# Kernel tuning notes

Measured on AMD Instinct MI355X. Metric: run time of the kernel, lower is better.

## Reference

```python
import jax, jax.numpy as jnp
import numpy as np

B, N, C = 4, 4096, 256
GROUPS = 50
M_SCALE = 10.0


def setup_inputs() -> dict:
    key = jax.random.key(0)
    ks = jax.random.split(key, 6)
    s = 0.02
    return {
        "inputs": jax.random.normal(ks[0], (B, N, 1, C), dtype=jnp.float32),
        "W_sem": jax.random.normal(ks[1], (C, 128), dtype=jnp.float32) * s,
        "b_sem": jnp.zeros((128,), jnp.float32),
        "W_seg": jax.random.normal(ks[2], (128, GROUPS), dtype=jnp.float32) * s,
        "b_seg": jnp.zeros((GROUPS,), jnp.float32),
        "W_sim": jax.random.normal(ks[3], (C, 128), dtype=jnp.float32) * s,
        "b_sim": jnp.zeros((128,), jnp.float32),
        "W_conf": jax.random.normal(ks[4], (C, 128), dtype=jnp.float32) * s,
        "b_conf": jnp.zeros((128,), jnp.float32),
        "W_cl": jax.random.normal(ks[5], (128, 1), dtype=jnp.float32) * s,
        "b_cl": jnp.zeros((1,), jnp.float32),
    }


def reference(inputs, W_sem, b_sem, W_seg, b_seg, W_sim, b_sim,
              W_conf, b_conf, W_cl, b_cl):
    # 1x1 Conv2D on [B, N, 1, C] == per-point dense layer on channels.
    x = inputs[:, :, 0, :]  # [B, N, C]

    # Semantic segmentation head
    Fsem = jnp.einsum('bnc,cd->bnd', x, W_sem) + b_sem          # [B, N, 128]
    ptssemseg_logits = jnp.einsum('bnd,dg->bng', Fsem, W_seg) + b_seg  # [B, N, G]
    ptssemseg = jax.nn.softmax(ptssemseg_logits, axis=-1)

    # Similarity head: pairwise squared distances of Fsim rows
    Fsim = jnp.einsum('bnc,cd->bnd', x, W_sim) + b_sim          # [B, N, 128]
    r = jnp.sum(Fsim * Fsim, axis=2)                             # [B, N]
    gram = jnp.einsum('bnd,bmd->bnm', Fsim, Fsim)                # [B, N, N]
    D = r[:, :, None] - 2.0 * gram + r[:, None, :]               # [B, N, N]
    simmat_logits = jnp.maximum(M_SCALE * D, 0.0)

    # Confidence head
    Fconf = jnp.einsum('bnc,cd->bnd', x, W_conf) + b_conf        # [B, N, 128]
    conf_logits = jnp.einsum('bnd,do->bno', Fconf, W_cl) + b_cl  # [B, N, 1]
    conf = jax.nn.sigmoid(conf_logits)

    return (ptssemseg, ptssemseg_logits, simmat_logits, conf, conf_logits)
```

## Files before the change

### kernel.cpp

```cpp
#include <hip/hip_runtime.h>
#include <cstdint>
#include <cstddef>

#define NN 4096
#define CC 256
#define GG 50
#define PB 32
#define JD 384

#define O_OUT1 819200
#define O_OUT2 1638400
#define O_OUT3 68747264
#define O_OUT4 68763648

__device__ __forceinline__ unsigned bf16b(float f) {
    unsigned u = __float_as_uint(f);
    return (u + 0x7FFFu + ((u >> 16) & 1u)) >> 16;
}
__device__ __forceinline__ float bf16f(short s) {
    return __uint_as_float(((unsigned)(unsigned short)s) << 16);
}

__global__ __launch_bounds__(256) void k_proj(
    const float* __restrict__ x,
    const float* __restrict__ Wsem, const float* __restrict__ bsem,
    const float* __restrict__ Wseg, const float* __restrict__ bseg,
    const float* __restrict__ Wsim, const float* __restrict__ bsim,
    const float* __restrict__ Wconf, const float* __restrict__ bconf,
    const float* __restrict__ Wcl, const float* __restrict__ bcl,
    unsigned* __restrict__ fsimu, float* __restrict__ rnorm,
    float* __restrict__ out0, float* __restrict__ out1,
    float* __restrict__ out3, float* __restrict__ out4)
{
    __shared__ float smem[15360];
    __shared__ float confl[PB], mxs[PB], sms[PB], rns[PB];

    float* xs  = smem;
    float* wch = smem + 9216;

    int t = threadIdx.x;
    int pbase = blockIdx.x * PB;
    if (t < PB) { confl[t] = 0.f; rns[t] = 0.f; }

    #pragma unroll 4
    for (int p = 0; p < PB; ++p)
        xs[t * 36 + p] = x[(size_t)(pbase + p) * CC + t];

    int tj = t & 31, tp = t >> 5;
    float acc[4][12];
    #pragma unroll
    for (int pp = 0; pp < 4; ++pp)
        #pragma unroll
        for (int jj = 0; jj < 12; ++jj) acc[pp][jj] = 0.f;

    for (int kc = 0; kc < 16; ++kc) {
        __syncthreads();
        #pragma unroll
        for (int i = 0; i < 8; ++i) {
            int idx = i * 256 + t;
            int k = idx >> 7, jj = idx & 127;
            int g = (kc * 16 + k) * 128 + jj;
            wch[k * JD +       jj] = Wsim[g];
            wch[k * JD + 128 + jj] = Wsem[g];
            wch[k * JD + 256 + jj] = Wconf[g];
        }
        __syncthreads();
        #pragma unroll
        for (int k = 0; k < 16; ++k) {
            const float* xp = &xs[(kc * 16 + k) * 36 + tp * 4];
            float a0 = xp[0], a1 = xp[1], a2 = xp[2], a3 = xp[3];
            const float* wr = &wch[k * JD + tj * 12];
            #pragma unroll
            for (int jj = 0; jj < 12; ++jj) {
                float w = wr[jj];
                acc[0][jj] = fmaf(a0, w, acc[0][jj]);
                acc[1][jj] = fmaf(a1, w, acc[1][jj]);
                acc[2][jj] = fmaf(a2, w, acc[2][jj]);
                acc[3][jj] = fmaf(a3, w, acc[3][jj]);
            }
        }
    }
    __syncthreads();

    float* hsem = smem;
    float* WsT  = smem + 4224;
    float* segl = smem + 10824;

    for (int i = t; i < GG * 128; i += 256) {
        int g = i >> 7, d = i & 127;
        WsT[g * 132 + d] = Wseg[d * GG + g];
    }

    #pragma unroll
    for (int pp = 0; pp < 4; ++pp) {
        int p = tp * 4 + pp;
        float vv[12];
        #pragma unroll
        for (int jj = 0; jj < 12; ++jj) {
            int j = tj * 12 + jj;
            float bb = (j < 128) ? bsim[j] : (j < 256 ? bsem[j - 128] : bconf[j - 256]);
            vv[jj] = acc[pp][jj] + bb;
        }
        float rsq = 0.f;
        #pragma unroll
        for (int jj = 0; jj < 12; ++jj) {
            int j = tj * 12 + jj;
            if (j < 128) {
                float f = bf16f((short)bf16b(vv[jj]));
                rsq = fmaf(f, f, rsq);
            }
        }
        if (tj <= 10) atomicAdd(&rns[p], rsq);
        #pragma unroll
        for (int jj = 0; jj < 12; jj += 2) {
            int j = tj * 12 + jj;
            if (j < 128)
                fsimu[(size_t)(pbase + p) * 64 + (j >> 1)] =
                    bf16b(vv[jj]) | (bf16b(vv[jj + 1]) << 16);
        }
        #pragma unroll
        for (int jj = 0; jj < 12; ++jj) {
            int j = tj * 12 + jj;
            if (j >= 128 && j < 256) hsem[p * 132 + (j - 128)] = vv[jj];
        }
        float c = 0.f;
        #pragma unroll
        for (int jj = 0; jj < 12; ++jj) {
            int j = tj * 12 + jj;
            if (j >= 256) c = fmaf(vv[jj], Wcl[j - 256], c);
        }
        if (tj >= 21) atomicAdd(&confl[p], c);
    }
    __syncthreads();

    for (int i = t; i < PB * GG; i += 256) {
        int p = i / GG, g = i - p * GG;
        const float4* hp = (const float4*)&hsem[p * 132];
        const float4* wp = (const float4*)&WsT[g * 132];
        float a = bseg[g];
        #pragma unroll 8
        for (int d = 0; d < 32; ++d) {
            float4 h = hp[d], w = wp[d];
            a = fmaf(h.x, w.x, a); a = fmaf(h.y, w.y, a);
            a = fmaf(h.z, w.z, a); a = fmaf(h.w, w.w, a);
        }
        segl[p * 52 + g] = a;
    }
    __syncthreads();

    if (t < PB) {
        int p = t;
        float mx = -1e30f;
        for (int g = 0; g < GG; ++g) mx = fmaxf(mx, segl[p * 52 + g]);
        float s = 0.f;
        for (int g = 0; g < GG; ++g) s += __expf(segl[p * 52 + g] - mx);
        mxs[p] = mx; sms[p] = 1.f / s;
        float cl = confl[p] + bcl[0];
        out4[pbase + p] = cl;
        out3[pbase + p] = 1.f / (1.f + __expf(-cl));
        rnorm[pbase + p] = rns[p];
    }
    __syncthreads();

    for (int i = t; i < PB * GG; i += 256) {
        int p = i / GG, g = i - p * GG;
        float l = segl[p * 52 + g];
        size_t o = (size_t)(pbase + p) * GG + g;
        out1[o] = l;
        out0[o] = __expf(l - mxs[p]) * sms[p];
    }
}

typedef short short8 __attribute__((ext_vector_type(8)));
typedef float f32x4 __attribute__((ext_vector_type(4)));

__global__ __launch_bounds__(256) void k_simmat(
    const short* __restrict__ fs, const float* __restrict__ rn, float* __restrict__ out2)
{
    int t = threadIdx.x;
    int lane = t & 63, wv = t >> 6;
    int b = blockIdx.y;

    int p = blockIdx.x;
    int tj = (int)((sqrtf((float)(8 * p + 1)) - 1.f) * 0.5f);
    while ((tj + 1) * (tj + 2) / 2 <= p) ++tj;
    while (tj * (tj + 1) / 2 > p) --tj;
    int ti = p - tj * (tj + 1) / 2;

    int I = ti * 128 + (wv >> 1) * 64;
    int J = tj * 128 + (wv & 1) * 64;
    int rowl = lane & 15, quad = lane >> 4;

    const short8* F = (const short8*)(fs + (size_t)b * NN * 128);
    const float* rb = rn + b * NN;

    f32x4 acc[4][4];
    #pragma unroll
    for (int r = 0; r < 4; ++r)
        #pragma unroll
        for (int c = 0; c < 4; ++c) { f32x4 z = {0.f,0.f,0.f,0.f}; acc[r][c] = z; }

    #pragma unroll
    for (int s = 0; s < 4; ++s) {
        short8 av[4], bv[4];
        #pragma unroll
        for (int r = 0; r < 4; ++r)
            av[r] = F[(size_t)(I + r * 16 + rowl) * 16 + s * 4 + quad];
        #pragma unroll
        for (int c = 0; c < 4; ++c)
            bv[c] = F[(size_t)(J + c * 16 + rowl) * 16 + s * 4 + quad];
        #pragma unroll
        for (int r = 0; r < 4; ++r)
            #pragma unroll
            for (int c = 0; c < 4; ++c)
                acc[r][c] = __builtin_amdgcn_mfma_f32_16x16x32_bf16(av[r], bv[c], acc[r][c], 0, 0, 0);
    }

    f32x4 rI4[4];
    float rJs[4];
    #pragma unroll
    for (int r = 0; r < 4; ++r)
        rI4[r] = *(const f32x4*)&rb[I + r * 16 + quad * 4];
    #pragma unroll
    for (int c = 0; c < 4; ++c)
        rJs[c] = rb[J + c * 16 + rowl];

    #pragma unroll
    for (int r = 0; r < 4; ++r)
        #pragma unroll
        for (int c = 0; c < 4; ++c) {
            f32x4 v = acc[r][c];
            float rj = rJs[c];
            f32x4 o;
            #pragma unroll
            for (int e = 0; e < 4; ++e)
                o[e] = fmaxf(10.f * (rI4[r][e] + rj) - 20.f * v[e], 0.f);
            acc[r][c] = o;
        }

    float* ob = out2 + (size_t)b * NN * NN;

    #pragma unroll
    for (int r = 0; r < 4; ++r) {
        int rbase = I + r * 16 + quad * 4;
        #pragma unroll
        for (int c = 0; c < 4; ++c) {
            int col = J + c * 16 + rowl;
            f32x4 v = acc[r][c];
            #pragma unroll
            for (int e = 0; e < 4; ++e)
                __builtin_nontemporal_store(v[e], &ob[(size_t)(rbase + e) * NN + col]);
        }
    }

    if (ti != tj) {
        #pragma unroll
        for (int c = 0; c < 4; ++c) {
            size_t rowoff = (size_t)(J + c * 16 + rowl) * NN;
            #pragma unroll
            for (int r = 0; r < 4; ++r)
                __builtin_nontemporal_store(acc[r][c],
                    (f32x4*)&ob[rowoff + (I + r * 16 + quad * 4)]);
        }
    }
}

extern "C" void kernel_launch(void* const* d_in, const int* in_sizes, int n_in,
                              void* d_out, int out_size, void* d_ws, size_t ws_size,
                              hipStream_t stream)
{
    const float* x     = (const float*)d_in[0];
    const float* Wsem  = (const float*)d_in[1];
    const float* bsem  = (const float*)d_in[2];
    const float* Wseg  = (const float*)d_in[3];
    const float* bseg  = (const float*)d_in[4];
    const float* Wsim  = (const float*)d_in[5];
    const float* bsim  = (const float*)d_in[6];
    const float* Wconf = (const float*)d_in[7];
    const float* bconf = (const float*)d_in[8];
    const float* Wcl   = (const float*)d_in[9];
    const float* bcl   = (const float*)d_in[10];

    const size_t FSIM_BYTES = (size_t)4 * NN * 128 * 2;
    if (ws_size < FSIM_BYTES + (size_t)4 * NN * sizeof(float)) return;
    unsigned* fsim = (unsigned*)d_ws;
    float* rnorm = (float*)((char*)d_ws + FSIM_BYTES);

    float* out  = (float*)d_out;
    float* out0 = out;
    float* out1 = out + O_OUT1;
    float* out2 = out + O_OUT2;
    float* out3 = out + O_OUT3;
    float* out4 = out + O_OUT4;

    hipLaunchKernelGGL(k_proj, dim3(512), dim3(256), 0, stream,
                       x, Wsem, bsem, Wseg, bseg, Wsim, bsim, Wconf, bconf, Wcl, bcl,
                       fsim, rnorm, out0, out1, out3, out4);
    hipLaunchKernelGGL(k_simmat, dim3(528, 4, 1), dim3(256), 0, stream,
                       (const short*)fsim, rnorm, out2);
}
```

Measured before the change: 422.7 us.

## Rewrite projection kernel with fp16 MFMA for dense layers and segmentation head

Replaces the scalar-FMA projection kernel with one that uses 16x16x32 fp16 MFMA for the three 256->128 projections, converting weights and inputs to half on load straight from global memory rather than staging them in shared memory. The segmentation logits are also computed with MFMA, and the softmax is done with wave shuffles instead of a single-thread loop. Block size grows to 64 points, giving 256 blocks. This lowers projection precision to fp16 and reads weights with strided uncached-pattern loads, and the projection kernel is likely a small share of total time next to the N×N simmat kernel.

```diff
diff --git a/kernel.cpp b/kernel.cpp
--- a/kernel.cpp
+++ b/kernel.cpp
@@ -5,13 +5,15 @@
 #define NN 4096
 #define CC 256
 #define GG 50
-#define PB 32
-#define JD 384
 
 #define O_OUT1 819200
 #define O_OUT2 1638400
 #define O_OUT3 68747264
 #define O_OUT4 68763648
+
+typedef _Float16 half8 __attribute__((ext_vector_type(8)));
+typedef float f32x4 __attribute__((ext_vector_type(4)));
+typedef short short8 __attribute__((ext_vector_type(8)));
 
 __device__ __forceinline__ unsigned bf16b(float f) {
     unsigned u = __float_as_uint(f);
@@ -32,147 +34,186 @@
     float* __restrict__ out0, float* __restrict__ out1,
     float* __restrict__ out3, float* __restrict__ out4)
 {
-    __shared__ float smem[15360];
-    __shared__ float confl[PB], mxs[PB], sms[PB], rns[PB];
-
-    float* xs  = smem;
-    float* wch = smem + 9216;
+    __shared__ float hsem[64 * 132];
+    __shared__ float confl[64], rns[64];
 
     int t = threadIdx.x;
-    int pbase = blockIdx.x * PB;
-    if (t < PB) { confl[t] = 0.f; rns[t] = 0.f; }
-
-    #pragma unroll 4
-    for (int p = 0; p < PB; ++p)
-        xs[t * 36 + p] = x[(size_t)(pbase + p) * CC + t];
-
-    int tj = t & 31, tp = t >> 5;
-    float acc[4][12];
-    #pragma unroll
-    for (int pp = 0; pp < 4; ++pp)
-        #pragma unroll
-        for (int jj = 0; jj < 12; ++jj) acc[pp][jj] = 0.f;
-
-    for (int kc = 0; kc < 16; ++kc) {
-        __syncthreads();
-        #pragma unroll
-        for (int i = 0; i < 8; ++i) {
-            int idx = i * 256 + t;
-            int k = idx >> 7, jj = idx & 127;
-            int g = (kc * 16 + k) * 128 + jj;
-            wch[k * JD +       jj] = Wsim[g];
-            wch[k * JD + 128 + jj] = Wsem[g];
-            wch[k * JD + 256 + jj] = Wconf[g];
-        }
-        __syncthreads();
-        #pragma unroll
-        for (int k = 0; k < 16; ++k) {
-            const float* xp = &xs[(kc * 16 + k) * 36 + tp * 4];
-            float a0 = xp[0], a1 = xp[1], a2 = xp[2], a3 = xp[3];
-            const float* wr = &wch[k * JD + tj * 12];
-            #pragma unroll
-            for (int jj = 0; jj < 12; ++jj) {
-                float w = wr[jj];
-                acc[0][jj] = fmaf(a0, w, acc[0][jj]);
-                acc[1][jj] = fmaf(a1, w, acc[1][jj]);
-                acc[2][jj] = fmaf(a2, w, acc[2][jj]);
-                acc[3][jj] = fmaf(a3, w, acc[3][jj]);
-            }
-        }
-    }
+    int lane = t & 63, wv = t >> 6;
+    int rowl = lane & 15, quad = lane >> 4;
+    int pbase = blockIdx.x * 64;
+
+    if (t < 64) { confl[t] = 0.f; rns[t] = 0.f; }
+
+    const float* wcol[6];
+    #pragma unroll
+    for (int jf = 0; jf < 6; ++jf) {
+        int j384 = (wv * 6 + jf) * 16 + rowl;
+        const float* m = (j384 < 128) ? Wsim : (j384 < 256) ? Wsem : Wconf;
+        wcol[jf] = m + (j384 & 127);
+    }
+    const float* xrow[4];
+    #pragma unroll
+    for (int pf = 0; pf < 4; ++pf)
+        xrow[pf] = x + (size_t)(pbase + pf * 16 + rowl) * CC;
+
+    f32x4 acc[6][4];
+    #pragma unroll
+    for (int jf = 0; jf < 6; ++jf)
+        #pragma unroll
+        for (int pf = 0; pf < 4; ++pf) { f32x4 z = {0.f,0.f,0.f,0.f}; acc[jf][pf] = z; }
+
+    #pragma unroll 2
+    for (int kc = 0; kc < 8; ++kc) {
+        half8 A[6];
+        #pragma unroll
+        for (int jf = 0; jf < 6; ++jf) {
+            const float* wp = wcol[jf] + (size_t)(kc * 32 + quad * 8) * 128;
+            #pragma unroll
+            for (int e = 0; e < 8; ++e) A[jf][e] = (_Float16)wp[(size_t)e * 128];
+        }
+        half8 Bv[4];
+        #pragma unroll
+        for (int pf = 0; pf < 4; ++pf) {
+            const float* xp = xrow[pf] + kc * 32 + quad * 8;
+            float4 x0 = *(const float4*)xp;
+            float4 x1 = *(const float4*)(xp + 4);
+            Bv[pf][0] = (_Float16)x0.x; Bv[pf][1] = (_Float16)x0.y;
+            Bv[pf][2] = (_Float16)x0.z; Bv[pf][3] = (_Float16)x0.w;
+            Bv[pf][4] = (_Float16)x1.x; Bv[pf][5] = (_Float16)x1.y;
+            Bv[pf][6] = (_Float16)x1.z; Bv[pf][7] = (_Float16)x1.w;
+        }
+        #pragma unroll
+        for (int pf = 0; pf < 4; ++pf)
+            #pragma unroll
+            for (int jf = 0; jf < 6; ++jf)
+                acc[jf][pf] = __builtin_amdgcn_mfma_f32_16x16x32_f16(A[jf], Bv[pf], acc[jf][pf], 0, 0, 0);
+    }
+
     __syncthreads();
 
-    float* hsem = smem;
-    float* WsT  = smem + 4224;
-    float* segl = smem + 10824;
-
-    for (int i = t; i < GG * 128; i += 256) {
-        int g = i >> 7, d = i & 127;
-        WsT[g * 132 + d] = Wseg[d * GG + g];
-    }
-
-    #pragma unroll
-    for (int pp = 0; pp < 4; ++pp) {
-        int p = tp * 4 + pp;
-        float vv[12];
-        #pragma unroll
-        for (int jj = 0; jj < 12; ++jj) {
-            int j = tj * 12 + jj;
-            float bb = (j < 128) ? bsim[j] : (j < 256 ? bsem[j - 128] : bconf[j - 256]);
-            vv[jj] = acc[pp][jj] + bb;
-        }
-        float rsq = 0.f;
-        #pragma unroll
-        for (int jj = 0; jj < 12; ++jj) {
-            int j = tj * 12 + jj;
-            if (j < 128) {
-                float f = bf16f((short)bf16b(vv[jj]));
-                rsq = fmaf(f, f, rsq);
-            }
-        }
-        if (tj <= 10) atomicAdd(&rns[p], rsq);
-        #pragma unroll
-        for (int jj = 0; jj < 12; jj += 2) {
-            int j = tj * 12 + jj;
-            if (j < 128)
-                fsimu[(size_t)(pbase + p) * 64 + (j >> 1)] =
-                    bf16b(vv[jj]) | (bf16b(vv[jj + 1]) << 16);
-        }
-        #pragma unroll
-        for (int jj = 0; jj < 12; ++jj) {
-            int j = tj * 12 + jj;
-            if (j >= 128 && j < 256) hsem[p * 132 + (j - 128)] = vv[jj];
-        }
-        float c = 0.f;
-        #pragma unroll
-        for (int jj = 0; jj < 12; ++jj) {
-            int j = tj * 12 + jj;
-            if (j >= 256) c = fmaf(vv[jj], Wcl[j - 256], c);
-        }
-        if (tj >= 21) atomicAdd(&confl[p], c);
+    float rsum[4] = {0.f,0.f,0.f,0.f};
+    float csum[4] = {0.f,0.f,0.f,0.f};
+    bool hasSim = (wv * 6 < 8);
+    bool hasConf = (wv * 6 + 5 >= 16);
+
+    #pragma unroll
+    for (int jf = 0; jf < 6; ++jf) {
+        int jfg = wv * 6 + jf;
+        int j0 = jfg * 16 + quad * 4;
+        const float* barr = (j0 < 128) ? (bsim + j0)
+                          : (j0 < 256) ? (bsem + (j0 - 128)) : (bconf + (j0 - 256));
+        float4 b4 = *(const float4*)barr;
+        if (jfg < 8) {
+            #pragma unroll
+            for (int pf = 0; pf < 4; ++pf) {
+                int pt = pf * 16 + rowl;
+                f32x4 v = acc[jf][pf];
+                unsigned p0 = bf16b(v[0] + b4.x) | (bf16b(v[1] + b4.y) << 16);
+                unsigned p1 = bf16b(v[2] + b4.z) | (bf16b(v[3] + b4.w) << 16);
+                *(uint2*)&fsimu[(size_t)(pbase + pt) * 64 + jfg * 8 + quad * 2] = make_uint2(p0, p1);
+                float f0 = bf16f((short)(p0 & 0xFFFF)), f1 = bf16f((short)(p0 >> 16));
+                float f2 = bf16f((short)(p1 & 0xFFFF)), f3 = bf16f((short)(p1 >> 16));
+                rsum[pf] += f0*f0 + f1*f1 + f2*f2 + f3*f3;
+            }
+        } else if (jfg < 16) {
+            #pragma unroll
+            for (int pf = 0; pf < 4; ++pf) {
+                int pt = pf * 16 + rowl;
+                f32x4 v = acc[jf][pf];
+                f32x4 o;
+                o[0] = v[0] + b4.x; o[1] = v[1] + b4.y; o[2] = v[2] + b4.z; o[3] = v[3] + b4.w;
+                *(f32x4*)&hsem[pt * 132 + (jfg - 8) * 16 + quad * 4] = o;
+            }
+        } else {
+            float4 w4 = *(const float4*)&Wcl[(jfg - 16) * 16 + quad * 4];
+            #pragma unroll
+            for (int pf = 0; pf < 4; ++pf) {
+                f32x4 v = acc[jf][pf];
+                csum[pf] += (v[0] + b4.x) * w4.x + (v[1] + b4.y) * w4.y
+                          + (v[2] + b4.z) * w4.z + (v[3] + b4.w) * w4.w;
+            }
+        }
+    }
+    if (hasSim) {
+        #pragma unroll
+        for (int pf = 0; pf < 4; ++pf) atomicAdd(&rns[pf * 16 + rowl], rsum[pf]);
+    }
+    if (hasConf) {
+        #pragma unroll
+        for (int pf = 0; pf < 4; ++pf) atomicAdd(&confl[pf * 16 + rowl], csum[pf]);
     }
     __syncthreads();
 
-    for (int i = t; i < PB * GG; i += 256) {
-        int p = i / GG, g = i - p * GG;
-        const float4* hp = (const float4*)&hsem[p * 132];
-        const float4* wp = (const float4*)&WsT[g * 132];
-        float a = bseg[g];
-        #pragma unroll 8
-        for (int d = 0; d < 32; ++d) {
-            float4 h = hp[d], w = wp[d];
-            a = fmaf(h.x, w.x, a); a = fmaf(h.y, w.y, a);
-            a = fmaf(h.z, w.z, a); a = fmaf(h.w, w.w, a);
-        }
-        segl[p * 52 + g] = a;
-    }
-    __syncthreads();
-
-    if (t < PB) {
-        int p = t;
-        float mx = -1e30f;
-        for (int g = 0; g < GG; ++g) mx = fmaxf(mx, segl[p * 52 + g]);
-        float s = 0.f;
-        for (int g = 0; g < GG; ++g) s += __expf(segl[p * 52 + g] - mx);
-        mxs[p] = mx; sms[p] = 1.f / s;
-        float cl = confl[p] + bcl[0];
-        out4[pbase + p] = cl;
-        out3[pbase + p] = 1.f / (1.f + __expf(-cl));
-        rnorm[pbase + p] = rns[p];
-    }
-    __syncthreads();
-
-    for (int i = t; i < PB * GG; i += 256) {
-        int p = i / GG, g = i - p * GG;
-        float l = segl[p * 52 + g];
-        size_t o = (size_t)(pbase + p) * GG + g;
-        out1[o] = l;
-        out0[o] = __expf(l - mxs[p]) * sms[p];
-    }
-}
-
-typedef short short8 __attribute__((ext_vector_type(8)));
-typedef float f32x4 __attribute__((ext_vector_type(4)));
+    if (t < 64) {
+        float cl = confl[t] + bcl[0];
+        out4[pbase + t] = cl;
+        out3[pbase + t] = 1.f / (1.f + __expf(-cl));
+        rnorm[pbase + t] = rns[t];
+    }
+
+    half8 As[4][4];
+    #pragma unroll
+    for (int gf = 0; gf < 4; ++gf) {
+        int gg = gf * 16 + rowl;
+        #pragma unroll
+        for (int k2 = 0; k2 < 4; ++k2)
+            #pragma unroll
+            for (int e = 0; e < 8; ++e) {
+                int d = k2 * 32 + quad * 8 + e;
+                As[gf][k2][e] = (gg < GG) ? (_Float16)Wseg[(size_t)d * GG + gg] : (_Float16)0.f;
+            }
+    }
+    f32x4 sacc[4];
+    #pragma unroll
+    for (int gf = 0; gf < 4; ++gf) { f32x4 z = {0.f,0.f,0.f,0.f}; sacc[gf] = z; }
+    #pragma unroll
+    for (int k2 = 0; k2 < 4; ++k2) {
+        const float* hp = &hsem[(wv * 16 + rowl) * 132 + k2 * 32 + quad * 8];
+        half8 Bh;
+        #pragma unroll
+        for (int e = 0; e < 8; ++e) Bh[e] = (_Float16)hp[e];
+        #pragma unroll
+        for (int gf = 0; gf < 4; ++gf)
+            sacc[gf] = __builtin_amdgcn_mfma_f32_16x16x32_f16(As[gf][k2], Bh, sacc[gf], 0, 0, 0);
+    }
+
+    float l[4][4];
+    float mx = -1e30f;
+    #pragma unroll
+    for (int gf = 0; gf < 4; ++gf)
+        #pragma unroll
+        for (int e = 0; e < 4; ++e) {
+            int g = gf * 16 + quad * 4 + e;
+            float lv = (g < GG) ? sacc[gf][e] + bseg[g] : -1e30f;
+            l[gf][e] = lv;
+            mx = fmaxf(mx, lv);
+        }
+    mx = fmaxf(mx, __shfl_xor(mx, 16));
+    mx = fmaxf(mx, __shfl_xor(mx, 32));
+    float s = 0.f;
+    #pragma unroll
+    for (int gf = 0; gf < 4; ++gf)
+        #pragma unroll
+        for (int e = 0; e < 4; ++e) {
+            int g = gf * 16 + quad * 4 + e;
+            if (g < GG) s += __expf(l[gf][e] - mx);
+        }
+    s += __shfl_xor(s, 16);
+    s += __shfl_xor(s, 32);
+    float inv = 1.f / s;
+
+    size_t orow = (size_t)(pbase + wv * 16 + rowl) * GG;
+    #pragma unroll
+    for (int gf = 0; gf < 4; ++gf)
+        #pragma unroll
+        for (int e = 0; e < 4; ++e) {
+            int g = gf * 16 + quad * 4 + e;
+            if (g < GG) {
+                out1[orow + g] = l[gf][e];
+                out0[orow + g] = __expf(l[gf][e] - mx) * inv;
+            }
+        }
+}
 
 __global__ __launch_bounds__(256) void k_simmat(
     const short* __restrict__ fs, const float* __restrict__ rn, float* __restrict__ out2)
@@ -293,7 +334,7 @@
     float* out3 = out + O_OUT3;
     float* out4 = out + O_OUT4;
 
-    hipLaunchKernelGGL(k_proj, dim3(512), dim3(256), 0, stream,
+    hipLaunchKernelGGL(k_proj, dim3(256), dim3(256), 0, stream,
                        x, Wsem, bsem, Wseg, bseg, Wsim, bsim, Wconf, bconf, Wcl, bcl,
                        fsim, rnorm, out0, out1, out3, out4);
     hipLaunchKernelGGL(k_simmat, dim3(528, 4, 1), dim3(256), 0, stream,
```

Result: faster. 357.9 us, median of 2 (-15.3%).
